# Performance work log

Hardware: AMD Instinct MI355X
Metric: run time of the kernel (lower is better)

The kernel has to match this reference:

```python
import math
import jax, jax.numpy as jnp
import numpy as np

B, S, HID = 1, 256, 1024
H, D = 16, 64
INV_NORM = 1.0 / math.sqrt(D)  # inv_norm_factor (beta = 1.0)
NEG = -1e9


def _bloom_alibi(num_heads, seq_len):
    # standard Bloom alibi slopes, shape [H, 1, S]
    closest_pow2 = 2 ** math.floor(math.log2(num_heads))
    base = 2.0 ** (-(2.0 ** -(math.log2(closest_pow2) - 3)))
    slopes = base ** np.arange(1, closest_pow2 + 1)
    if closest_pow2 != num_heads:
        extra_base = 2.0 ** (-(2.0 ** -(math.log2(2 * closest_pow2) - 3)))
        n_extra = min(closest_pow2, num_heads - closest_pow2)
        slopes = np.concatenate([slopes, extra_base ** np.arange(1, 1 + 2 * n_extra, 2)])
    pos = np.arange(seq_len, dtype=np.float32)[None, None, :]
    return jnp.asarray(slopes[:, None, None].astype(np.float32) * pos)  # [H,1,S]


def setup_inputs() -> dict:
    key = jax.random.key(0)
    ks = jax.random.split(key, 6)
    hidden_states = jax.random.normal(ks[0], (B, S, HID), jnp.float32)
    residual = jax.random.normal(ks[1], (B, S, HID), jnp.float32)
    alibi = _bloom_alibi(H, S)  # [B*H, 1, S] with B=1
    # additive causal mask [B, 1, S, S]
    causal = jnp.tril(jnp.ones((S, S), bool))
    attention_mask = jnp.where(causal, 0.0, NEG).astype(jnp.float32)[None, None]
    W_qkv = jax.random.normal(ks[2], (HID, 3 * HID), jnp.float32) * (1.0 / math.sqrt(HID))
    b_qkv = jax.random.normal(ks[3], (3 * HID,), jnp.float32) * 0.02
    W_dense = jax.random.normal(ks[4], (HID, HID), jnp.float32) * (1.0 / math.sqrt(HID))
    b_dense = jax.random.normal(ks[5], (HID,), jnp.float32) * 0.02
    return dict(hidden_states=hidden_states, residual=residual, alibi=alibi,
                attention_mask=attention_mask, W_qkv=W_qkv, b_qkv=b_qkv,
                W_dense=W_dense, b_dense=b_dense)


def reference(hidden_states, residual, alibi, attention_mask, W_qkv, b_qkv, W_dense, b_dense):
    b, s, _ = hidden_states.shape
    # fused qkv projection, Bloom layout: (B, S, H, 3, D)
    fused = (hidden_states @ W_qkv + b_qkv).reshape(b, s, H, 3, D)
    q = fused[..., 0, :].transpose(0, 2, 1, 3)  # [B,H,S,D]
    k = fused[..., 1, :].transpose(0, 2, 1, 3)
    v = fused[..., 2, :].transpose(0, 2, 1, 3)

    alibi_b = alibi.reshape(b, H, 1, s)  # broadcast over query dim
    # standard alibi attention scores: [B,H,S,S]
    scores = alibi_b + INV_NORM * jnp.einsum('bhid,bhjd->bhij', q, k)
    scores = scores + attention_mask  # mask applied only to full scores (as in source)
    # per-dim delta scores: [B,H,D,S,S]; delta[b,h,d,i,j] = alibi + inv_norm * q_d * k_d
    delta = alibi_b[:, :, None] + INV_NORM * jnp.einsum('bhid,bhjd->bhdij', q, k)

    diff = (scores[:, :, None] - delta) * (1.0 / math.sqrt(D))
    p_diff = jax.nn.softmax(diff.astype(jnp.float32), axis=-1)  # [B,H,D,S,S]
    p = jax.nn.softmax(scores.astype(jnp.float32), axis=-1)     # [B,H,S,S]

    # qk importance: sum over batch, query, key of squared deviation, per (h, d)
    qk_importance = jnp.sum((p_diff - p[:, :, None]) ** 2, axis=(0, 3, 4)).reshape(-1)  # [H*D]

    context = jnp.einsum('bhij,bhjd->bhid', p, v)  # [B,H,S,D]
    context = context.transpose(0, 2, 1, 3).reshape(b, s, H * D)
    out = context @ W_dense + b_dense
    out = out + residual  # eval mode: dropout is identity
    return out, qk_importance
```

## Files before the change

kernel.cpp:

```cpp
#include <hip/hip_runtime.h>
#include <math.h>

#define NH  16
#define SEQ 256
#define HD  64
#define HID 1024
#define N3  3072

#define OFF_QB   0
#define OFF_KB   131072
#define OFF_KTB  262144
#define OFF_VTB  393216
#define OFF_CTX  524288

typedef __attribute__((ext_vector_type(8))) short bf16x8;
typedef __attribute__((ext_vector_type(4))) float f32x4;
typedef __attribute__((ext_vector_type(4))) unsigned short us4;
typedef __attribute__((ext_vector_type(8))) unsigned short us8;

__device__ __forceinline__ unsigned short f2bf(float x) {
  unsigned u = __builtin_bit_cast(unsigned, x);
  u += 0x7FFF + ((u >> 16) & 1);
  return (unsigned short)(u >> 16);
}
__device__ __forceinline__ float bf2f(unsigned short b) {
  return __builtin_bit_cast(float, (unsigned)b << 16);
}

__global__ __launch_bounds__(256) void k_qkv(
    const float* __restrict__ A, const float* __restrict__ W,
    const float* __restrict__ bias, float* __restrict__ ws,
    float* __restrict__ out) {
  if (blockIdx.x == 0 && blockIdx.y < 4)
    out[SEQ * HID + blockIdx.y * 256 + threadIdx.x] = 0.f;
  __shared__ __align__(16) unsigned short As[64 * 40];
  __shared__ __align__(16) unsigned short Bs[64 * 40];
  const int tid = threadIdx.x;
  const int w = tid >> 6, lane = tid & 63;
  const int m0 = blockIdx.y * 64, n0 = blockIdx.x * 64;
  const int am = tid >> 3, ak = (tid & 7) * 4;
  const int bkg = w * 8;
  const float* Wp = W + n0 + lane;
  float4 a0 = *(const float4*)&A[(m0 + am) * HID + ak];
  float4 a1 = *(const float4*)&A[(m0 + 32 + am) * HID + ak];
  float pb[8];
#pragma unroll
  for (int u = 0; u < 8; ++u) pb[u] = Wp[(bkg + u) * N3];
  f32x4 acc[4] = {{0.f, 0.f, 0.f, 0.f}, {0.f, 0.f, 0.f, 0.f},
                  {0.f, 0.f, 0.f, 0.f}, {0.f, 0.f, 0.f, 0.f}};
  const int col = lane & 15, quad = lane >> 4;
  const int k8 = quad * 8;
  for (int k0 = 0; k0 < HID; k0 += 32) {
    *(us4*)&As[am * 40 + ak] =
        (us4){f2bf(a0.x), f2bf(a0.y), f2bf(a0.z), f2bf(a0.w)};
    *(us4*)&As[(am + 32) * 40 + ak] =
        (us4){f2bf(a1.x), f2bf(a1.y), f2bf(a1.z), f2bf(a1.w)};
    us8 bp;
#pragma unroll
    for (int u = 0; u < 8; ++u) bp[u] = f2bf(pb[u]);
    *(us8*)&Bs[lane * 40 + bkg] = bp;
    __syncthreads();
    const int kn = k0 + 32;
    if (kn < HID) {
      a0 = *(const float4*)&A[(m0 + am) * HID + kn + ak];
      a1 = *(const float4*)&A[(m0 + 32 + am) * HID + kn + ak];
#pragma unroll
      for (int u = 0; u < 8; ++u) pb[u] = Wp[(kn + bkg + u) * N3];
    }
    const bf16x8 af = *(const bf16x8*)&As[(w * 16 + col) * 40 + k8];
#pragma unroll
    for (int t = 0; t < 4; ++t) {
      const bf16x8 bf = *(const bf16x8*)&Bs[(t * 16 + col) * 40 + k8];
      acc[t] = __builtin_amdgcn_mfma_f32_16x16x32_bf16(af, bf, acc[t], 0, 0, 0);
    }
    __syncthreads();
  }
  unsigned short* qb  = (unsigned short*)(ws + OFF_QB);
  unsigned short* kb  = (unsigned short*)(ws + OFF_KB);
  unsigned short* ktb = (unsigned short*)(ws + OFF_KTB);
  unsigned short* vtb = (unsigned short*)(ws + OFF_VTB);
#pragma unroll
  for (int t = 0; t < 4; ++t) {
    const int n = n0 + t * 16 + col;
    const int h = n / 192;
    const int r2 = n - h * 192;
    const int which = r2 >> 6, d = r2 & 63;
    const float bv = bias[n];
#pragma unroll
    for (int r = 0; r < 4; ++r) {
      const int m = m0 + w * 16 + quad * 4 + r;
      const unsigned short vb = f2bf(acc[t][r] + bv);
      if (which == 0) {
        qb[(h * SEQ + m) * HD + d] = vb;
      } else if (which == 1) {
        kb[(h * SEQ + m) * HD + d] = vb;
        ktb[(h * HD + d) * SEQ + m] = vb;
      } else {
        vtb[(h * HD + d) * SEQ + m] = vb;
      }
    }
  }
}

__global__ __launch_bounds__(256) void k_attn(
    const float* __restrict__ alibi, float* __restrict__ ws,
    float* __restrict__ out) {
  const int bx = blockIdx.x;
  const int h = bx >> 4, i0 = (bx & 15) * 16;
  const int tid = threadIdx.x, w = tid >> 6, lane = tid & 63;
  const int col = lane & 15, quad = lane >> 4;
  __shared__ __align__(16) unsigned short Albs[3 * 16 * 280];
  __shared__ __align__(16) float plds[16 * 260];
  __shared__ __align__(16) float redm[16][4];
  __shared__ __align__(16) float reds[16][4];
  __shared__ __align__(16) float red4[16][4][4];
  __shared__ __align__(16) float rowsc[16][4];
  const unsigned short* qb  = (const unsigned short*)(ws + OFF_QB) + h * SEQ * HD;
  const unsigned short* kb  = (const unsigned short*)(ws + OFF_KB) + h * SEQ * HD;
  const unsigned short* ktb = (const unsigned short*)(ws + OFF_KTB) + h * HD * SEQ;
  const unsigned short* vtb = (const unsigned short*)(ws + OFF_VTB) + h * HD * SEQ;
  const bf16x8 a0 = *(const bf16x8*)&qb[(i0 + col) * HD + quad * 8];
  const bf16x8 a1 = *(const bf16x8*)&qb[(i0 + col) * HD + quad * 8 + 32];
  f32x4 acc[4] = {{0.f, 0.f, 0.f, 0.f}, {0.f, 0.f, 0.f, 0.f},
                  {0.f, 0.f, 0.f, 0.f}, {0.f, 0.f, 0.f, 0.f}};
#pragma unroll
  for (int t = 0; t < 4; ++t) {
    const int j = w * 64 + t * 16 + col;
    const bf16x8 b0 = *(const bf16x8*)&kb[j * HD + quad * 8];
    const bf16x8 b1 = *(const bf16x8*)&kb[j * HD + quad * 8 + 32];
    acc[t] = __builtin_amdgcn_mfma_f32_16x16x32_bf16(a0, b0, acc[t], 0, 0, 0);
    acc[t] = __builtin_amdgcn_mfma_f32_16x16x32_bf16(a1, b1, acc[t], 0, 0, 0);
  }
  float c[4][4], eb[4][4];
  float rmax[4] = {-3.0e38f, -3.0e38f, -3.0e38f, -3.0e38f};
#pragma unroll
  for (int t = 0; t < 4; ++t) {
    const int j = w * 64 + t * 16 + col;
    const float al = alibi[h * SEQ + j];
#pragma unroll
    for (int r = 0; r < 4; ++r) {
      const int i = i0 + quad * 4 + r;
      const float s = acc[t][r] * 0.125f;
      const float mv = (j <= i) ? 0.f : -1e9f;
      eb[t][r] = __expf((s + mv) * 0.125f);
      const float cv = al + s + mv;
      c[t][r] = cv;
      rmax[r] = fmaxf(rmax[r], cv);
    }
  }
#pragma unroll
  for (int r = 0; r < 4; ++r)
#pragma unroll
    for (int off = 1; off < 16; off <<= 1)
      rmax[r] = fmaxf(rmax[r], __shfl_xor(rmax[r], off));
  if (col == 0)
#pragma unroll
    for (int r = 0; r < 4; ++r) redm[quad * 4 + r][w] = rmax[r];
  __syncthreads();
  float rsum[4];
#pragma unroll
  for (int r = 0; r < 4; ++r) {
    const float4 m4 = *(const float4*)redm[quad * 4 + r];
    const float M = fmaxf(fmaxf(m4.x, m4.y), fmaxf(m4.z, m4.w));
    float s = 0.f;
#pragma unroll
    for (int t = 0; t < 4; ++t) {
      c[t][r] = __expf(c[t][r] - M);
      s += c[t][r];
    }
#pragma unroll
    for (int off = 1; off < 16; off <<= 1) s += __shfl_xor(s, off);
    rsum[r] = s;
  }
  if (col == 0)
#pragma unroll
    for (int r = 0; r < 4; ++r) reds[quad * 4 + r][w] = rsum[r];
  __syncthreads();
#pragma unroll
  for (int r = 0; r < 4; ++r) {
    const float4 s4 = *(const float4*)reds[quad * 4 + r];
    const float inv = __builtin_amdgcn_rcpf((s4.x + s4.y) + (s4.z + s4.w));
    const int il = quad * 4 + r;
    float s0 = 0.f, t0 = 0.f, u0 = 0.f, sp = 0.f;
#pragma unroll
    for (int t = 0; t < 4; ++t) {
      const int j = w * 64 + t * 16 + col;
      const float p = c[t][r] * inv;
      const float E = eb[t][r];
      plds[il * 260 + j] = p;
      Albs[il * 280 + j] = f2bf(E);
      Albs[16 * 280 + il * 280 + j] = f2bf(E * E);
      Albs[2 * 16 * 280 + il * 280 + j] = f2bf(E * p);
      s0 += E;
      t0 = __builtin_fmaf(E, E, t0);
      u0 = __builtin_fmaf(E, p, u0);
      sp = __builtin_fmaf(p, p, sp);
    }
#pragma unroll
    for (int off = 1; off < 16; off <<= 1) {
      s0 += __shfl_xor(s0, off);
      t0 += __shfl_xor(t0, off);
      u0 += __shfl_xor(u0, off);
      sp += __shfl_xor(sp, off);
    }
    if (col == 0) *(float4*)&red4[il][w][0] = (float4){s0, t0, u0, sp};
  }
  __syncthreads();
  if (tid < 64) {
    const int row = tid >> 2, x = tid & 3;
    rowsc[row][x] = (red4[row][0][x] + red4[row][1][x]) +
                    (red4[row][2][x] + red4[row][3][x]);
  }
  __syncthreads();
  f32x4 o = {0.f, 0.f, 0.f, 0.f};
#pragma unroll
  for (int s = 0; s < 8; ++s) {
    const int k8 = quad * 8 + s * 32;
    const float4 pa = *(const float4*)&plds[col * 260 + k8];
    const float4 pc = *(const float4*)&plds[col * 260 + k8 + 4];
    const us8 af = {f2bf(pa.x), f2bf(pa.y), f2bf(pa.z), f2bf(pa.w),
                    f2bf(pc.x), f2bf(pc.y), f2bf(pc.z), f2bf(pc.w)};
    const bf16x8 vb = *(const bf16x8*)&vtb[(w * 16 + col) * SEQ + k8];
    o = __builtin_amdgcn_mfma_f32_16x16x32_bf16(
        __builtin_bit_cast(bf16x8, af), vb, o, 0, 0, 0);
  }
  float* ctx = ws + OFF_CTX;
#pragma unroll
  for (int r = 0; r < 4; ++r)
    ctx[(i0 + quad * 4 + r) * HID + h * HD + w * 16 + col] = o[r];
  f32x4 m6[3][2] = {{{0.f, 0.f, 0.f, 0.f}, {0.f, 0.f, 0.f, 0.f}},
                    {{0.f, 0.f, 0.f, 0.f}, {0.f, 0.f, 0.f, 0.f}},
                    {{0.f, 0.f, 0.f, 0.f}, {0.f, 0.f, 0.f, 0.f}}};
  const unsigned short* ktrow = ktb + (w * 16 + col) * SEQ;
#pragma unroll
  for (int s = 0; s < 8; ++s) {
    const int kk = quad * 8 + s * 32;
    const bf16x8 kb8 = *(const bf16x8*)&ktrow[kk];
    us8 kq;
#pragma unroll
    for (int u = 0; u < 8; ++u) {
      const float t = bf2f((unsigned short)kb8[u]);
      kq[u] = f2bf(t * t);
    }
    const bf16x8 k2 = __builtin_bit_cast(bf16x8, kq);
#pragma unroll
    for (int lhs = 0; lhs < 3; ++lhs) {
      const bf16x8 af = *(const bf16x8*)&Albs[lhs * 16 * 280 + col * 280 + kk];
      m6[lhs][0] = __builtin_amdgcn_mfma_f32_16x16x32_bf16(af, kb8, m6[lhs][0], 0, 0, 0);
      m6[lhs][1] = __builtin_amdgcn_mfma_f32_16x16x32_bf16(af, k2, m6[lhs][1], 0, 0, 0);
    }
  }
  const int dg = w * 16 + col;
  float racc = 0.f;
#pragma unroll
  for (int r = 0; r < 4; ++r) {
    const int il = quad * 4 + r;
    const float qc = -0.015625f * bf2f(qb[(i0 + il) * HD + dg]);
    const float s0 = rowsc[il][0], t0 = rowsc[il][1];
    const float u0 = rowsc[il][2], sp = rowsc[il][3];
    const float S1 = __builtin_fmaf(
        qc, __builtin_fmaf(0.5f * qc, m6[0][1][r], m6[0][0][r]), s0);
    const float S2 = __builtin_fmaf(
        2.f * qc, __builtin_fmaf(qc, m6[1][1][r], m6[1][0][r]), t0);
    const float S3 = __builtin_fmaf(
        qc, __builtin_fmaf(0.5f * qc, m6[2][1][r], m6[2][0][r]), u0);
    const float inv = __builtin_amdgcn_rcpf(S1);
    racc += __builtin_fmaf(__builtin_fmaf(S2, inv, -2.f * S3), inv, sp);
  }
  racc += __shfl_xor(racc, 16);
  racc += __shfl_xor(racc, 32);
  if (lane < 16) atomicAdd(&out[SEQ * HID + h * HD + w * 16 + lane], racc);
}

__global__ __launch_bounds__(256) void k_dense(
    const float* __restrict__ W, const float* __restrict__ bias,
    const float* __restrict__ resid, float* __restrict__ out,
    const float* __restrict__ ws) {
  __shared__ __align__(16) unsigned short As[32 * 40];
  __shared__ __align__(16) unsigned short Bs[64 * 40];
  const int tid = threadIdx.x;
  const int w = tid >> 6, lane = tid & 63;
  const int m0 = blockIdx.y * 32, n0 = blockIdx.x * 64;
  const int am = tid >> 3, ak = (tid & 7) * 4;
  const int bkg = w * 8;
  const float* A = ws + OFF_CTX;
  const float* Wp = W + n0 + lane;
  float4 a0 = *(const float4*)&A[(m0 + am) * HID + ak];
  float pb[8];
#pragma unroll
  for (int u = 0; u < 8; ++u) pb[u] = Wp[(bkg + u) * HID];
  f32x4 acc[2] = {{0.f, 0.f, 0.f, 0.f}, {0.f, 0.f, 0.f, 0.f}};
  const int col = lane & 15, quad = lane >> 4;
  const int k8 = quad * 8;
  const int mt = w & 1, nh = w >> 1;
  for (int k0 = 0; k0 < HID; k0 += 32) {
    *(us4*)&As[am * 40 + ak] =
        (us4){f2bf(a0.x), f2bf(a0.y), f2bf(a0.z), f2bf(a0.w)};
    us8 bp;
#pragma unroll
    for (int u = 0; u < 8; ++u) bp[u] = f2bf(pb[u]);
    *(us8*)&Bs[lane * 40 + bkg] = bp;
    __syncthreads();
    const int kn = k0 + 32;
    if (kn < HID) {
      a0 = *(const float4*)&A[(m0 + am) * HID + kn + ak];
#pragma unroll
      for (int u = 0; u < 8; ++u) pb[u] = Wp[(kn + bkg + u) * HID];
    }
    const bf16x8 af = *(const bf16x8*)&As[(mt * 16 + col) * 40 + k8];
#pragma unroll
    for (int t = 0; t < 2; ++t) {
      const bf16x8 bf =
          *(const bf16x8*)&Bs[(nh * 32 + t * 16 + col) * 40 + k8];
      acc[t] = __builtin_amdgcn_mfma_f32_16x16x32_bf16(af, bf, acc[t], 0, 0, 0);
    }
    __syncthreads();
  }
#pragma unroll
  for (int t = 0; t < 2; ++t) {
    const int n = n0 + nh * 32 + t * 16 + col;
    const float bv = bias[n];
#pragma unroll
    for (int r = 0; r < 4; ++r) {
      const int m = m0 + mt * 16 + quad * 4 + r;
      out[m * HID + n] = acc[t][r] + bv + resid[m * HID + n];
    }
  }
}

extern "C" void kernel_launch(void* const* d_in, const int* in_sizes, int n_in,
                              void* d_out, int out_size, void* d_ws,
                              size_t ws_size, hipStream_t stream) {
  const float* hidden   = (const float*)d_in[0];
  const float* residual = (const float*)d_in[1];
  const float* alibi    = (const float*)d_in[2];
  const float* Wqkv     = (const float*)d_in[4];
  const float* bqkv     = (const float*)d_in[5];
  const float* Wd       = (const float*)d_in[6];
  const float* bd       = (const float*)d_in[7];
  float* out = (float*)d_out;
  float* ws  = (float*)d_ws;

  k_qkv<<<dim3(48, 4), 256, 0, stream>>>(hidden, Wqkv, bqkv, ws, out);
  k_attn<<<dim3(256), 256, 0, stream>>>(alibi, ws, out);
  k_dense<<<dim3(16, 8), 256, 0, stream>>>(Wd, bd, residual, out, ws);
}
```

Baseline: 128.2 us.

## Fuse QKV, attention and dense kernels into one cooperative kernel with grid syncs

```diff
diff --git a/kernel.cpp b/kernel.cpp
--- a/kernel.cpp
+++ b/kernel.cpp
@@ -1,5 +1,8 @@
 #include <hip/hip_runtime.h>
+#include <hip/hip_cooperative_groups.h>
 #include <math.h>
+
+namespace cg = cooperative_groups;
 
 #define NH  16
 #define SEQ 256
@@ -27,303 +30,304 @@
   return __builtin_bit_cast(float, (unsigned)b << 16);
 }
 
-__global__ __launch_bounds__(256) void k_qkv(
+__global__ __launch_bounds__(256) void k_fused(
     const float* __restrict__ A, const float* __restrict__ W,
-    const float* __restrict__ bias, float* __restrict__ ws,
+    const float* __restrict__ bias, const float* __restrict__ alibi,
+    const float* __restrict__ Wd, const float* __restrict__ bd,
+    const float* __restrict__ resid, float* __restrict__ ws,
     float* __restrict__ out) {
-  if (blockIdx.x == 0 && blockIdx.y < 4)
-    out[SEQ * HID + blockIdx.y * 256 + threadIdx.x] = 0.f;
-  __shared__ __align__(16) unsigned short As[64 * 40];
-  __shared__ __align__(16) unsigned short Bs[64 * 40];
+  cg::grid_group grid = cg::this_grid();
+  __shared__ __align__(16) char smem[45312];
+  const int bid = blockIdx.x;
   const int tid = threadIdx.x;
   const int w = tid >> 6, lane = tid & 63;
-  const int m0 = blockIdx.y * 64, n0 = blockIdx.x * 64;
-  const int am = tid >> 3, ak = (tid & 7) * 4;
-  const int bkg = w * 8;
-  const float* Wp = W + n0 + lane;
-  float4 a0 = *(const float4*)&A[(m0 + am) * HID + ak];
-  float4 a1 = *(const float4*)&A[(m0 + 32 + am) * HID + ak];
-  float pb[8];
-#pragma unroll
-  for (int u = 0; u < 8; ++u) pb[u] = Wp[(bkg + u) * N3];
-  f32x4 acc[4] = {{0.f, 0.f, 0.f, 0.f}, {0.f, 0.f, 0.f, 0.f},
-                  {0.f, 0.f, 0.f, 0.f}, {0.f, 0.f, 0.f, 0.f}};
   const int col = lane & 15, quad = lane >> 4;
-  const int k8 = quad * 8;
-  for (int k0 = 0; k0 < HID; k0 += 32) {
-    *(us4*)&As[am * 40 + ak] =
-        (us4){f2bf(a0.x), f2bf(a0.y), f2bf(a0.z), f2bf(a0.w)};
-    *(us4*)&As[(am + 32) * 40 + ak] =
-        (us4){f2bf(a1.x), f2bf(a1.y), f2bf(a1.z), f2bf(a1.w)};
-    us8 bp;
-#pragma unroll
-    for (int u = 0; u < 8; ++u) bp[u] = f2bf(pb[u]);
-    *(us8*)&Bs[lane * 40 + bkg] = bp;
-    __syncthreads();
-    const int kn = k0 + 32;
-    if (kn < HID) {
-      a0 = *(const float4*)&A[(m0 + am) * HID + kn + ak];
-      a1 = *(const float4*)&A[(m0 + 32 + am) * HID + kn + ak];
-#pragma unroll
-      for (int u = 0; u < 8; ++u) pb[u] = Wp[(kn + bkg + u) * N3];
-    }
-    const bf16x8 af = *(const bf16x8*)&As[(w * 16 + col) * 40 + k8];
-#pragma unroll
-    for (int t = 0; t < 4; ++t) {
-      const bf16x8 bf = *(const bf16x8*)&Bs[(t * 16 + col) * 40 + k8];
-      acc[t] = __builtin_amdgcn_mfma_f32_16x16x32_bf16(af, bf, acc[t], 0, 0, 0);
-    }
-    __syncthreads();
-  }
   unsigned short* qb  = (unsigned short*)(ws + OFF_QB);
   unsigned short* kb  = (unsigned short*)(ws + OFF_KB);
   unsigned short* ktb = (unsigned short*)(ws + OFF_KTB);
   unsigned short* vtb = (unsigned short*)(ws + OFF_VTB);
-#pragma unroll
-  for (int t = 0; t < 4; ++t) {
-    const int n = n0 + t * 16 + col;
-    const int h = n / 192;
-    const int r2 = n - h * 192;
-    const int which = r2 >> 6, d = r2 & 63;
-    const float bv = bias[n];
-#pragma unroll
-    for (int r = 0; r < 4; ++r) {
-      const int m = m0 + w * 16 + quad * 4 + r;
-      const unsigned short vb = f2bf(acc[t][r] + bv);
-      if (which == 0) {
-        qb[(h * SEQ + m) * HD + d] = vb;
-      } else if (which == 1) {
-        kb[(h * SEQ + m) * HD + d] = vb;
-        ktb[(h * HD + d) * SEQ + m] = vb;
-      } else {
-        vtb[(h * HD + d) * SEQ + m] = vb;
-      }
-    }
+  float* ctx = ws + OFF_CTX;
+
+  if (bid < 192) {
+    unsigned short* As = (unsigned short*)smem;
+    unsigned short* Bs = As + 64 * 40;
+    const int m0 = (bid / 48) * 64, n0 = (bid % 48) * 64;
+    const int am = tid >> 3, ak = (tid & 7) * 4;
+    const int bkg = w * 8;
+    const float* Wp = W + n0 + lane;
+    float4 a0 = *(const float4*)&A[(m0 + am) * HID + ak];
+    float4 a1 = *(const float4*)&A[(m0 + 32 + am) * HID + ak];
+    float pb[8];
+#pragma unroll
+    for (int u = 0; u < 8; ++u) pb[u] = Wp[(bkg + u) * N3];
+    f32x4 acc[4] = {{0.f, 0.f, 0.f, 0.f}, {0.f, 0.f, 0.f, 0.f},
+                    {0.f, 0.f, 0.f, 0.f}, {0.f, 0.f, 0.f, 0.f}};
+    const int k8 = quad * 8;
+    for (int k0 = 0; k0 < HID; k0 += 32) {
+      *(us4*)&As[am * 40 + ak] =
+          (us4){f2bf(a0.x), f2bf(a0.y), f2bf(a0.z), f2bf(a0.w)};
+      *(us4*)&As[(am + 32) * 40 + ak] =
+          (us4){f2bf(a1.x), f2bf(a1.y), f2bf(a1.z), f2bf(a1.w)};
+      us8 bp;
+#pragma unroll
+      for (int u = 0; u < 8; ++u) bp[u] = f2bf(pb[u]);
+      *(us8*)&Bs[lane * 40 + bkg] = bp;
+      __syncthreads();
+      const int kn = k0 + 32;
+      if (kn < HID) {
+        a0 = *(const float4*)&A[(m0 + am) * HID + kn + ak];
+        a1 = *(const float4*)&A[(m0 + 32 + am) * HID + kn + ak];
+#pragma unroll
+        for (int u = 0; u < 8; ++u) pb[u] = Wp[(kn + bkg + u) * N3];
+      }
+      const bf16x8 af = *(const bf16x8*)&As[(w * 16 + col) * 40 + k8];
+#pragma unroll
+      for (int t = 0; t < 4; ++t) {
+        const bf16x8 bf = *(const bf16x8*)&Bs[(t * 16 + col) * 40 + k8];
+        acc[t] = __builtin_amdgcn_mfma_f32_16x16x32_bf16(af, bf, acc[t], 0, 0, 0);
+      }
+      __syncthreads();
+    }
+#pragma unroll
+    for (int t = 0; t < 4; ++t) {
+      const int n = n0 + t * 16 + col;
+      const int h = n / 192;
+      const int r2 = n - h * 192;
+      const int which = r2 >> 6, d = r2 & 63;
+      const float bv = bias[n];
+#pragma unroll
+      for (int r = 0; r < 4; ++r) {
+        const int m = m0 + w * 16 + quad * 4 + r;
+        const unsigned short vb = f2bf(acc[t][r] + bv);
+        if (which == 0) {
+          qb[(h * SEQ + m) * HD + d] = vb;
+        } else if (which == 1) {
+          kb[(h * SEQ + m) * HD + d] = vb;
+          ktb[(h * HD + d) * SEQ + m] = vb;
+        } else {
+          vtb[(h * HD + d) * SEQ + m] = vb;
+        }
+      }
+    }
+  } else if (bid < 196) {
+    out[SEQ * HID + (bid - 192) * 256 + tid] = 0.f;
   }
-}
-
-__global__ __launch_bounds__(256) void k_attn(
-    const float* __restrict__ alibi, float* __restrict__ ws,
-    float* __restrict__ out) {
-  const int bx = blockIdx.x;
-  const int h = bx >> 4, i0 = (bx & 15) * 16;
-  const int tid = threadIdx.x, w = tid >> 6, lane = tid & 63;
-  const int col = lane & 15, quad = lane >> 4;
-  __shared__ __align__(16) unsigned short Albs[3 * 16 * 280];
-  __shared__ __align__(16) float plds[16 * 260];
-  __shared__ __align__(16) float redm[16][4];
-  __shared__ __align__(16) float reds[16][4];
-  __shared__ __align__(16) float red4[16][4][4];
-  __shared__ __align__(16) float rowsc[16][4];
-  const unsigned short* qb  = (const unsigned short*)(ws + OFF_QB) + h * SEQ * HD;
-  const unsigned short* kb  = (const unsigned short*)(ws + OFF_KB) + h * SEQ * HD;
-  const unsigned short* ktb = (const unsigned short*)(ws + OFF_KTB) + h * HD * SEQ;
-  const unsigned short* vtb = (const unsigned short*)(ws + OFF_VTB) + h * HD * SEQ;
-  const bf16x8 a0 = *(const bf16x8*)&qb[(i0 + col) * HD + quad * 8];
-  const bf16x8 a1 = *(const bf16x8*)&qb[(i0 + col) * HD + quad * 8 + 32];
-  f32x4 acc[4] = {{0.f, 0.f, 0.f, 0.f}, {0.f, 0.f, 0.f, 0.f},
-                  {0.f, 0.f, 0.f, 0.f}, {0.f, 0.f, 0.f, 0.f}};
-#pragma unroll
-  for (int t = 0; t < 4; ++t) {
-    const int j = w * 64 + t * 16 + col;
-    const bf16x8 b0 = *(const bf16x8*)&kb[j * HD + quad * 8];
-    const bf16x8 b1 = *(const bf16x8*)&kb[j * HD + quad * 8 + 32];
-    acc[t] = __builtin_amdgcn_mfma_f32_16x16x32_bf16(a0, b0, acc[t], 0, 0, 0);
-    acc[t] = __builtin_amdgcn_mfma_f32_16x16x32_bf16(a1, b1, acc[t], 0, 0, 0);
-  }
-  float c[4][4], eb[4][4];
-  float rmax[4] = {-3.0e38f, -3.0e38f, -3.0e38f, -3.0e38f};
-#pragma unroll
-  for (int t = 0; t < 4; ++t) {
-    const int j = w * 64 + t * 16 + col;
-    const float al = alibi[h * SEQ + j];
-#pragma unroll
-    for (int r = 0; r < 4; ++r) {
-      const int i = i0 + quad * 4 + r;
-      const float s = acc[t][r] * 0.125f;
-      const float mv = (j <= i) ? 0.f : -1e9f;
-      eb[t][r] = __expf((s + mv) * 0.125f);
-      const float cv = al + s + mv;
-      c[t][r] = cv;
-      rmax[r] = fmaxf(rmax[r], cv);
-    }
-  }
-#pragma unroll
-  for (int r = 0; r < 4; ++r)
-#pragma unroll
-    for (int off = 1; off < 16; off <<= 1)
-      rmax[r] = fmaxf(rmax[r], __shfl_xor(rmax[r], off));
-  if (col == 0)
-#pragma unroll
-    for (int r = 0; r < 4; ++r) redm[quad * 4 + r][w] = rmax[r];
-  __syncthreads();
-  float rsum[4];
-#pragma unroll
-  for (int r = 0; r < 4; ++r) {
-    const float4 m4 = *(const float4*)redm[quad * 4 + r];
-    const float M = fmaxf(fmaxf(m4.x, m4.y), fmaxf(m4.z, m4.w));
-    float s = 0.f;
-#pragma unroll
-    for (int t = 0; t < 4; ++t) {
-      c[t][r] = __expf(c[t][r] - M);
-      s += c[t][r];
-    }
-#pragma unroll
-    for (int off = 1; off < 16; off <<= 1) s += __shfl_xor(s, off);
-    rsum[r] = s;
-  }
-  if (col == 0)
-#pragma unroll
-    for (int r = 0; r < 4; ++r) reds[quad * 4 + r][w] = rsum[r];
-  __syncthreads();
-#pragma unroll
-  for (int r = 0; r < 4; ++r) {
-    const float4 s4 = *(const float4*)reds[quad * 4 + r];
-    const float inv = __builtin_amdgcn_rcpf((s4.x + s4.y) + (s4.z + s4.w));
-    const int il = quad * 4 + r;
-    float s0 = 0.f, t0 = 0.f, u0 = 0.f, sp = 0.f;
+  __threadfence();
+  grid.sync();
+
+  {
+    const int h = bid >> 4, i0 = (bid & 15) * 16;
+    unsigned short* Albs = (unsigned short*)smem;
+    float* plds  = (float*)(smem + 26880);
+    float* redm  = (float*)(smem + 43520);
+    float* reds  = (float*)(smem + 43776);
+    float* red4  = (float*)(smem + 44032);
+    float* rowsc = (float*)(smem + 45056);
+    const unsigned short* qbh  = qb + h * SEQ * HD;
+    const unsigned short* kbh  = kb + h * SEQ * HD;
+    const unsigned short* ktbh = ktb + h * HD * SEQ;
+    const unsigned short* vtbh = vtb + h * HD * SEQ;
+    const bf16x8 a0 = *(const bf16x8*)&qbh[(i0 + col) * HD + quad * 8];
+    const bf16x8 a1 = *(const bf16x8*)&qbh[(i0 + col) * HD + quad * 8 + 32];
+    f32x4 acc[4] = {{0.f, 0.f, 0.f, 0.f}, {0.f, 0.f, 0.f, 0.f},
+                    {0.f, 0.f, 0.f, 0.f}, {0.f, 0.f, 0.f, 0.f}};
 #pragma unroll
     for (int t = 0; t < 4; ++t) {
       const int j = w * 64 + t * 16 + col;
-      const float p = c[t][r] * inv;
-      const float E = eb[t][r];
-      plds[il * 260 + j] = p;
-      Albs[il * 280 + j] = f2bf(E);
-      Albs[16 * 280 + il * 280 + j] = f2bf(E * E);
-      Albs[2 * 16 * 280 + il * 280 + j] = f2bf(E * p);
-      s0 += E;
-      t0 = __builtin_fmaf(E, E, t0);
-      u0 = __builtin_fmaf(E, p, u0);
-      sp = __builtin_fmaf(p, p, sp);
-    }
-#pragma unroll
-    for (int off = 1; off < 16; off <<= 1) {
-      s0 += __shfl_xor(s0, off);
-      t0 += __shfl_xor(t0, off);
-      u0 += __shfl_xor(u0, off);
-      sp += __shfl_xor(sp, off);
-    }
-    if (col == 0) *(float4*)&red4[il][w][0] = (float4){s0, t0, u0, sp};
+      const bf16x8 b0 = *(const bf16x8*)&kbh[j * HD + quad * 8];
+      const bf16x8 b1 = *(const bf16x8*)&kbh[j * HD + quad * 8 + 32];
+      acc[t] = __builtin_amdgcn_mfma_f32_16x16x32_bf16(a0, b0, acc[t], 0, 0, 0);
+      acc[t] = __builtin_amdgcn_mfma_f32_16x16x32_bf16(a1, b1, acc[t], 0, 0, 0);
+    }
+    float c[4][4], eb[4][4];
+    float rmax[4] = {-3.0e38f, -3.0e38f, -3.0e38f, -3.0e38f};
+#pragma unroll
+    for (int t = 0; t < 4; ++t) {
+      const int j = w * 64 + t * 16 + col;
+      const float al = alibi[h * SEQ + j];
+#pragma unroll
+      for (int r = 0; r < 4; ++r) {
+        const int i = i0 + quad * 4 + r;
+        const float s = acc[t][r] * 0.125f;
+        const float mv = (j <= i) ? 0.f : -1e9f;
+        eb[t][r] = __expf((s + mv) * 0.125f);
+        const float cv = al + s + mv;
+        c[t][r] = cv;
+        rmax[r] = fmaxf(rmax[r], cv);
+      }
+    }
+#pragma unroll
+    for (int r = 0; r < 4; ++r)
+#pragma unroll
+      for (int off = 1; off < 16; off <<= 1)
+        rmax[r] = fmaxf(rmax[r], __shfl_xor(rmax[r], off));
+    if (col == 0)
+#pragma unroll
+      for (int r = 0; r < 4; ++r) redm[(quad * 4 + r) * 4 + w] = rmax[r];
+    __syncthreads();
+    float rsum[4];
+#pragma unroll
+    for (int r = 0; r < 4; ++r) {
+      const float4 m4 = *(const float4*)&redm[(quad * 4 + r) * 4];
+      const float M = fmaxf(fmaxf(m4.x, m4.y), fmaxf(m4.z, m4.w));
+      float s = 0.f;
+#pragma unroll
+      for (int t = 0; t < 4; ++t) {
+        c[t][r] = __expf(c[t][r] - M);
+        s += c[t][r];
+      }
+#pragma unroll
+      for (int off = 1; off < 16; off <<= 1) s += __shfl_xor(s, off);
+      rsum[r] = s;
+    }
+    if (col == 0)
+#pragma unroll
+      for (int r = 0; r < 4; ++r) reds[(quad * 4 + r) * 4 + w] = rsum[r];
+    __syncthreads();
+#pragma unroll
+    for (int r = 0; r < 4; ++r) {
+      const float4 s4 = *(const float4*)&reds[(quad * 4 + r) * 4];
+      const float inv = __builtin_amdgcn_rcpf((s4.x + s4.y) + (s4.z + s4.w));
+      const int il = quad * 4 + r;
+      float s0 = 0.f, t0 = 0.f, u0 = 0.f, sp = 0.f;
+#pragma unroll
+      for (int t = 0; t < 4; ++t) {
+        const int j = w * 64 + t * 16 + col;
+        const float p = c[t][r] * inv;
+        const float E = eb[t][r];
+        plds[il * 260 + j] = p;
+        Albs[il * 280 + j] = f2bf(E);
+        Albs[16 * 280 + il * 280 + j] = f2bf(E * E);
+        Albs[2 * 16 * 280 + il * 280 + j] = f2bf(E * p);
+        s0 += E;
+        t0 = __builtin_fmaf(E, E, t0);
+        u0 = __builtin_fmaf(E, p, u0);
+        sp = __builtin_fmaf(p, p, sp);
+      }
+#pragma unroll
+      for (int off = 1; off < 16; off <<= 1) {
+        s0 += __shfl_xor(s0, off);
+        t0 += __shfl_xor(t0, off);
+        u0 += __shfl_xor(u0, off);
+        sp += __shfl_xor(sp, off);
+      }
+      if (col == 0)
+        *(float4*)&red4[(il * 4 + w) * 4] = (float4){s0, t0, u0, sp};
+    }
+    __syncthreads();
+    if (tid < 64) {
+      const int row = tid >> 2, x = tid & 3;
+      rowsc[row * 4 + x] = (red4[(row * 4 + 0) * 4 + x] + red4[(row * 4 + 1) * 4 + x]) +
+                           (red4[(row * 4 + 2) * 4 + x] + red4[(row * 4 + 3) * 4 + x]);
+    }
+    __syncthreads();
+    f32x4 o = {0.f, 0.f, 0.f, 0.f};
+#pragma unroll
+    for (int s = 0; s < 8; ++s) {
+      const int kk = quad * 8 + s * 32;
+      const float4 pa = *(const float4*)&plds[col * 260 + kk];
+      const float4 pc = *(const float4*)&plds[col * 260 + kk + 4];
+      const us8 af = {f2bf(pa.x), f2bf(pa.y), f2bf(pa.z), f2bf(pa.w),
+                      f2bf(pc.x), f2bf(pc.y), f2bf(pc.z), f2bf(pc.w)};
+      const bf16x8 vb = *(const bf16x8*)&vtbh[(w * 16 + col) * SEQ + kk];
+      o = __builtin_amdgcn_mfma_f32_16x16x32_bf16(
+          __builtin_bit_cast(bf16x8, af), vb, o, 0, 0, 0);
+    }
+#pragma unroll
+    for (int r = 0; r < 4; ++r)
+      ctx[(i0 + quad * 4 + r) * HID + h * HD + w * 16 + col] = o[r];
+    f32x4 m6[3][2] = {{{0.f, 0.f, 0.f, 0.f}, {0.f, 0.f, 0.f, 0.f}},
+                      {{0.f, 0.f, 0.f, 0.f}, {0.f, 0.f, 0.f, 0.f}},
+                      {{0.f, 0.f, 0.f, 0.f}, {0.f, 0.f, 0.f, 0.f}}};
+    const unsigned short* ktrow = ktbh + (w * 16 + col) * SEQ;
+#pragma unroll
+    for (int s = 0; s < 8; ++s) {
+      const int kk = quad * 8 + s * 32;
+      const bf16x8 kb8 = *(const bf16x8*)&ktrow[kk];
+      us8 kq;
+#pragma unroll
+      for (int u = 0; u < 8; ++u) {
+        const float t = bf2f((unsigned short)kb8[u]);
+        kq[u] = f2bf(t * t);
+      }
+      const bf16x8 k2 = __builtin_bit_cast(bf16x8, kq);
+#pragma unroll
+      for (int lhs = 0; lhs < 3; ++lhs) {
+        const bf16x8 af = *(const bf16x8*)&Albs[lhs * 16 * 280 + col * 280 + kk];
+        m6[lhs][0] = __builtin_amdgcn_mfma_f32_16x16x32_bf16(af, kb8, m6[lhs][0], 0, 0, 0);
+        m6[lhs][1] = __builtin_amdgcn_mfma_f32_16x16x32_bf16(af, k2, m6[lhs][1], 0, 0, 0);
+      }
+    }
+    const int dg = w * 16 + col;
+    float racc = 0.f;
+#pragma unroll
+    for (int r = 0; r < 4; ++r) {
+      const int il = quad * 4 + r;
+      const float qc = -0.015625f * bf2f(qbh[(i0 + il) * HD + dg]);
+      const float s0 = rowsc[il * 4 + 0], t0 = rowsc[il * 4 + 1];
+      const float u0 = rowsc[il * 4 + 2], sp = rowsc[il * 4 + 3];
+      const float S1 = __builtin_fmaf(
+          qc, __builtin_fmaf(0.5f * qc, m6[0][1][r], m6[0][0][r]), s0);
+      const float S2 = __builtin_fmaf(
+          2.f * qc, __builtin_fmaf(qc, m6[1][1][r], m6[1][0][r]), t0);
+      const float S3 = __builtin_fmaf(
+          qc, __builtin_fmaf(0.5f * qc, m6[2][1][r], m6[2][0][r]), u0);
+      const float inv = __builtin_amdgcn_rcpf(S1);
+      racc += __builtin_fmaf(__builtin_fmaf(S2, inv, -2.f * S3), inv, sp);
+    }
+    racc += __shfl_xor(racc, 16);
+    racc += __shfl_xor(racc, 32);
+    if (lane < 16) atomicAdd(&out[SEQ * HID + h * HD + w * 16 + lane], racc);
   }
-  __syncthreads();
-  if (tid < 64) {
-    const int row = tid >> 2, x = tid & 3;
-    rowsc[row][x] = (red4[row][0][x] + red4[row][1][x]) +
-                    (red4[row][2][x] + red4[row][3][x]);
-  }
-  __syncthreads();
-  f32x4 o = {0.f, 0.f, 0.f, 0.f};
-#pragma unroll
-  for (int s = 0; s < 8; ++s) {
-    const int k8 = quad * 8 + s * 32;
-    const float4 pa = *(const float4*)&plds[col * 260 + k8];
-    const float4 pc = *(const float4*)&plds[col * 260 + k8 + 4];
-    const us8 af = {f2bf(pa.x), f2bf(pa.y), f2bf(pa.z), f2bf(pa.w),
-                    f2bf(pc.x), f2bf(pc.y), f2bf(pc.z), f2bf(pc.w)};
-    const bf16x8 vb = *(const bf16x8*)&vtb[(w * 16 + col) * SEQ + k8];
-    o = __builtin_amdgcn_mfma_f32_16x16x32_bf16(
-        __builtin_bit_cast(bf16x8, af), vb, o, 0, 0, 0);
-  }
-  float* ctx = ws + OFF_CTX;
-#pragma unroll
-  for (int r = 0; r < 4; ++r)
-    ctx[(i0 + quad * 4 + r) * HID + h * HD + w * 16 + col] = o[r];
-  f32x4 m6[3][2] = {{{0.f, 0.f, 0.f, 0.f}, {0.f, 0.f, 0.f, 0.f}},
-                    {{0.f, 0.f, 0.f, 0.f}, {0.f, 0.f, 0.f, 0.f}},
-                    {{0.f, 0.f, 0.f, 0.f}, {0.f, 0.f, 0.f, 0.f}}};
-  const unsigned short* ktrow = ktb + (w * 16 + col) * SEQ;
-#pragma unroll
-  for (int s = 0; s < 8; ++s) {
-    const int kk = quad * 8 + s * 32;
-    const bf16x8 kb8 = *(const bf16x8*)&ktrow[kk];
-    us8 kq;
-#pragma unroll
-    for (int u = 0; u < 8; ++u) {
-      const float t = bf2f((unsigned short)kb8[u]);
-      kq[u] = f2bf(t * t);
-    }
-    const bf16x8 k2 = __builtin_bit_cast(bf16x8, kq);
-#pragma unroll
-    for (int lhs = 0; lhs < 3; ++lhs) {
-      const bf16x8 af = *(const bf16x8*)&Albs[lhs * 16 * 280 + col * 280 + kk];
-      m6[lhs][0] = __builtin_amdgcn_mfma_f32_16x16x32_bf16(af, kb8, m6[lhs][0], 0, 0, 0);
-      m6[lhs][1] = __builtin_amdgcn_mfma_f32_16x16x32_bf16(af, k2, m6[lhs][1], 0, 0, 0);
-    }
-  }
-  const int dg = w * 16 + col;
-  float racc = 0.f;
-#pragma unroll
-  for (int r = 0; r < 4; ++r) {
-    const int il = quad * 4 + r;
-    const float qc = -0.015625f * bf2f(qb[(i0 + il) * HD + dg]);
-    const float s0 = rowsc[il][0], t0 = rowsc[il][1];
-    const float u0 = rowsc[il][2], sp = rowsc[il][3];
-    const float S1 = __builtin_fmaf(
-        qc, __builtin_fmaf(0.5f * qc, m6[0][1][r], m6[0][0][r]), s0);
-    const float S2 = __builtin_fmaf(
-        2.f * qc, __builtin_fmaf(qc, m6[1][1][r], m6[1][0][r]), t0);
-    const float S3 = __builtin_fmaf(
-        qc, __builtin_fmaf(0.5f * qc, m6[2][1][r], m6[2][0][r]), u0);
-    const float inv = __builtin_amdgcn_rcpf(S1);
-    racc += __builtin_fmaf(__builtin_fmaf(S2, inv, -2.f * S3), inv, sp);
-  }
-  racc += __shfl_xor(racc, 16);
-  racc += __shfl_xor(racc, 32);
-  if (lane < 16) atomicAdd(&out[SEQ * HID + h * HD + w * 16 + lane], racc);
-}
-
-__global__ __launch_bounds__(256) void k_dense(
-    const float* __restrict__ W, const float* __restrict__ bias,
-    const float* __restrict__ resid, float* __restrict__ out,
-    const float* __restrict__ ws) {
-  __shared__ __align__(16) unsigned short As[32 * 40];
-  __shared__ __align__(16) unsigned short Bs[64 * 40];
-  const int tid = threadIdx.x;
-  const int w = tid >> 6, lane = tid & 63;
-  const int m0 = blockIdx.y * 32, n0 = blockIdx.x * 64;
-  const int am = tid >> 3, ak = (tid & 7) * 4;
-  const int bkg = w * 8;
-  const float* A = ws + OFF_CTX;
-  const float* Wp = W + n0 + lane;
-  float4 a0 = *(const float4*)&A[(m0 + am) * HID + ak];
-  float pb[8];
-#pragma unroll
-  for (int u = 0; u < 8; ++u) pb[u] = Wp[(bkg + u) * HID];
-  f32x4 acc[2] = {{0.f, 0.f, 0.f, 0.f}, {0.f, 0.f, 0.f, 0.f}};
-  const int col = lane & 15, quad = lane >> 4;
-  const int k8 = quad * 8;
-  const int mt = w & 1, nh = w >> 1;
-  for (int k0 = 0; k0 < HID; k0 += 32) {
-    *(us4*)&As[am * 40 + ak] =
-        (us4){f2bf(a0.x), f2bf(a0.y), f2bf(a0.z), f2bf(a0.w)};
-    us8 bp;
-#pragma unroll
-    for (int u = 0; u < 8; ++u) bp[u] = f2bf(pb[u]);
-    *(us8*)&Bs[lane * 40 + bkg] = bp;
-    __syncthreads();
-    const int kn = k0 + 32;
-    if (kn < HID) {
-      a0 = *(const float4*)&A[(m0 + am) * HID + kn + ak];
-#pragma unroll
-      for (int u = 0; u < 8; ++u) pb[u] = Wp[(kn + bkg + u) * HID];
-    }
-    const bf16x8 af = *(const bf16x8*)&As[(mt * 16 + col) * 40 + k8];
+  __threadfence();
+  grid.sync();
+
+  if (bid < 128) {
+    unsigned short* As = (unsigned short*)smem;
+    unsigned short* Bs = As + 32 * 40;
+    const int m0 = (bid >> 4) * 32, n0 = (bid & 15) * 64;
+    const int am = tid >> 3, ak = (tid & 7) * 4;
+    const int bkg = w * 8;
+    const float* Wp = Wd + n0 + lane;
+    float4 a0 = *(const float4*)&ctx[(m0 + am) * HID + ak];
+    float pb[8];
+#pragma unroll
+    for (int u = 0; u < 8; ++u) pb[u] = Wp[(bkg + u) * HID];
+    f32x4 acc[2] = {{0.f, 0.f, 0.f, 0.f}, {0.f, 0.f, 0.f, 0.f}};
+    const int k8 = quad * 8;
+    const int mt = w & 1, nh = w >> 1;
+    for (int k0 = 0; k0 < HID; k0 += 32) {
+      *(us4*)&As[am * 40 + ak] =
+          (us4){f2bf(a0.x), f2bf(a0.y), f2bf(a0.z), f2bf(a0.w)};
+      us8 bp;
+#pragma unroll
+      for (int u = 0; u < 8; ++u) bp[u] = f2bf(pb[u]);
+      *(us8*)&Bs[lane * 40 + bkg] = bp;
+      __syncthreads();
+      const int kn = k0 + 32;
+      if (kn < HID) {
+        a0 = *(const float4*)&ctx[(m0 + am) * HID + kn + ak];
+#pragma unroll
+        for (int u = 0; u < 8; ++u) pb[u] = Wp[(kn + bkg + u) * HID];
+      }
+      const bf16x8 af = *(const bf16x8*)&As[(mt * 16 + col) * 40 + k8];
+#pragma unroll
+      for (int t = 0; t < 2; ++t) {
+        const bf16x8 bf =
+            *(const bf16x8*)&Bs[(nh * 32 + t * 16 + col) * 40 + k8];
+        acc[t] = __builtin_amdgcn_mfma_f32_16x16x32_bf16(af, bf, acc[t], 0, 0, 0);
+      }
+      __syncthreads();
+    }
 #pragma unroll
     for (int t = 0; t < 2; ++t) {
-      const bf16x8 bf =
-          *(const bf16x8*)&Bs[(nh * 32 + t * 16 + col) * 40 + k8];
-      acc[t] = __builtin_amdgcn_mfma_f32_16x16x32_bf16(af, bf, acc[t], 0, 0, 0);
-    }
-    __syncthreads();
-  }
-#pragma unroll
-  for (int t = 0; t < 2; ++t) {
-    const int n = n0 + nh * 32 + t * 16 + col;
-    const float bv = bias[n];
-#pragma unroll
-    for (int r = 0; r < 4; ++r) {
-      const int m = m0 + mt * 16 + quad * 4 + r;
-      out[m * HID + n] = acc[t][r] + bv + resid[m * HID + n];
+      const int n = n0 + nh * 32 + t * 16 + col;
+      const float bv = bd[n];
+#pragma unroll
+      for (int r = 0; r < 4; ++r) {
+        const int m = m0 + mt * 16 + quad * 4 + r;
+        out[m * HID + n] = acc[t][r] + bv + resid[m * HID + n];
+      }
     }
   }
 }
@@ -341,7 +345,9 @@
   float* out = (float*)d_out;
   float* ws  = (float*)d_ws;
 
-  k_qkv<<<dim3(48, 4), 256, 0, stream>>>(hidden, Wqkv, bqkv, ws, out);
-  k_attn<<<dim3(256), 256, 0, stream>>>(alibi, ws, out);
-  k_dense<<<dim3(16, 8), 256, 0, stream>>>(Wd, bd, residual, out, ws);
+  void* args[] = {(void*)&hidden, (void*)&Wqkv, (void*)&bqkv, (void*)&alibi,
+                  (void*)&Wd, (void*)&bd, (void*)&residual, (void*)&ws,
+                  (void*)&out};
+  hipLaunchCooperativeKernel((void*)k_fused, dim3(256), dim3(256), args, 0,
+                             stream);
 }
```

Measured after the change: 260.5 us. +103.1%, slower.
